# Kernel optimization log

Hardware: AMD Instinct MI355X
Metric: run time of the kernel (lower is better)

Reference implementation:

```python
import jax, jax.numpy as jnp
import numpy as np

ALPHA = 0.2   # LeakyReLU slope
V = 7         # graph nodes (hard-coded 7x7 adjacency in source)
BN_EPS = 1e-5


def _leaky(x):
    return jnp.where(x >= 0, x, ALPHA * x)


def _norm_adj(B):
    # adj = min-max normalized (B + I), then D^{-1/2} adj D^{-1/2}
    adj = B + jnp.eye(V, dtype=B.dtype)
    adj = (adj - adj.min()) / (adj.max() - adj.min())
    inv = 1.0 / jnp.sqrt(jnp.sum(adj, axis=1))
    return adj * inv[:, None] * inv[None, :]


def _gat1_head(h_flat, W, a, B):
    # h_flat: (N, V, C*T)=  (N,7,180); W: (180,9); a: (18,1); B: (7,7)
    Wh = h_flat @ W                       # (N, V, E)
    E = W.shape[1]
    s_i = Wh @ a[:E, 0]                   # (N, V)  == [Wh_i ; .] part of concat score
    s_j = Wh @ a[E:, 0]                   # (N, V)  == [. ; Wh_j] part
    e = _leaky(s_i[:, :, None] + s_j[:, None, :])   # (N, V, V)
    att = jax.nn.softmax(e, axis=-1)
    adjn = _norm_adj(B)
    att = jnp.einsum('ik,nkj->nij', adjn, att)      # adj_norm @ attention
    return jax.nn.elu(att @ Wh)           # (N, V, E)


def _gat2_head(h, W, a, B):
    # h: (N, V, C, 30); W: (30,10); a: (20,1); B: (7,7)
    Wh = h @ W                            # (N, V, C, F)
    F = W.shape[1]
    s_i = jnp.einsum('nvcf,f->nvc', Wh, a[:F, 0])
    s_j = jnp.einsum('nvcf,f->nvc', Wh, a[F:, 0])
    e = _leaky(s_i[:, :, None, :] + s_j[:, None, :, :])   # (N, V, V, C)
    att = jax.nn.softmax(e, axis=-1)      # softmax over channel dim (as in source)
    # nested V-loop with diag_embed == weighted sum over j, per-channel scaling
    h2 = jnp.einsum('njcf,nijc->ncfi', Wh, att)           # (N, C, F, V)
    adjn = _norm_adj(B)
    out = jnp.einsum('ncfu,uv->ncfv', h2, adjn)
    return jax.nn.elu(out)                # (N, C, F, V)


def setup_inputs() -> dict:
    key = jax.random.key(0)
    ks = jax.random.split(key, 16)
    N, C, T = 32768, 6, 30
    f32 = jnp.float32
    inp = {
        'x': jax.random.normal(ks[0], (N, C, T, V), f32),
        'bn_gamma': jax.random.uniform(ks[1], (42,), f32, 0.5, 1.5),
        'bn_beta': 0.1 * jax.random.normal(ks[2], (42,), f32),
        'W1': 0.1 * jax.random.normal(ks[3], (20, 180, 9), f32),
        'a1': 0.1 * jax.random.normal(ks[4], (20, 18, 1), f32),
        'B1': 0.01 * jax.random.uniform(ks[5], (20, V, V), f32) + 1e-6,
        'W2': 0.1 * jax.random.normal(ks[6], (3, 30, 10), f32),
        'a2': 0.1 * jax.random.normal(ks[7], (3, 20, 1), f32),
        'B2': 0.01 * jax.random.uniform(ks[8], (3, V, V), f32) + 1e-6,
        'W_ih': 0.1 * jax.random.normal(ks[9], (84, 84), f32),
        'W_hh': 0.1 * jax.random.normal(ks[10], (84, 21), f32),
        'b_ih': 0.1 * jax.random.normal(ks[11], (84,), f32),
        'b_hh': 0.1 * jax.random.normal(ks[12], (84,), f32),
        'W_out': 0.1 * jax.random.normal(ks[13], (7, 21), f32),
        'b_out': 0.1 * jax.random.normal(ks[14], (7,), f32),
    }
    return inp


def reference(x, bn_gamma, bn_beta, W1, a1, B1, W2, a2, B2,
              W_ih, W_hh, b_ih, b_hh, W_out, b_out):
    N, C, T, _ = x.shape                  # (N, 6, 30, 7)
    # data_bn: BatchNorm1d(42) in train mode (batch stats over N and T)
    xb = jnp.transpose(x, (0, 3, 1, 2)).reshape(N, V * C, T)
    mean = jnp.mean(xb, axis=(0, 2), keepdims=True)
    var = jnp.var(xb, axis=(0, 2), keepdims=True)
    xb = (xb - mean) / jnp.sqrt(var + BN_EPS)
    xb = xb * bn_gamma[None, :, None] + bn_beta[None, :, None]
    x0 = jnp.transpose(xb.reshape(N, V, C, T), (0, 2, 3, 1))   # (N, C, T, V)

    # l1: 20-head GAT on flattened (C*T) node features
    h_flat = jnp.transpose(x0, (0, 3, 1, 2)).reshape(N, V, C * T)
    heads1 = jax.vmap(_gat1_head, in_axes=(None, 0, 0, 0))(h_flat, W1, a1, B1)  # (20,N,V,9)
    x1 = jnp.moveaxis(heads1, 0, 2).reshape(N, V, C * T)       # cat over heads, last dim
    x1 = jnp.transpose(x1.reshape(N, V, C, T), (0, 2, 3, 1))   # (N, C, T, V)

    # l2: 3-head 2D GAT over the T axis
    h2in = jnp.transpose(x0, (0, 3, 1, 2))                      # (N, V, C, T)
    heads2 = jax.vmap(_gat2_head, in_axes=(None, 0, 0, 0))(h2in, W2, a2, B2)  # (3,N,C,10,V)
    x2 = jnp.moveaxis(heads2, 0, 2).reshape(N, C, 30, V)        # cat over heads on dim=2

    xcat = jnp.concatenate([x1, x2], axis=1)                    # (N, 12, 30, 7)

    # RNN head: source takes r_out[:, 0, :], so only LSTM step 0 (h0=c0=0) matters
    xs = jnp.transpose(xcat, (0, 2, 1, 3)).reshape(N, T, 84)
    gates = xs[:, 0, :] @ W_ih.T + b_ih + b_hh                  # h0=0 => W_hh term vanishes
    i_g, f_g, g_g, o_g = jnp.split(gates, 4, axis=-1)           # torch gate order i,f,g,o
    c1 = jax.nn.sigmoid(i_g) * jnp.tanh(g_g)
    h1 = jax.nn.sigmoid(o_g) * jnp.tanh(c1)
    return h1 @ W_out.T + b_out                                 # (N, 7)
```

## Files before the change

### kernel.cpp

```cpp
#include <hip/hip_runtime.h>

#define F1260 1260

__device__ __forceinline__ float leakyf(float x) { return x >= 0.f ? x : 0.2f * x; }
__device__ __forceinline__ float eluf(float x) { return x > 0.f ? x : expm1f(x); }
__device__ __forceinline__ float sigmoidf(float x) { return 1.f / (1.f + __expf(-x)); }
__device__ __forceinline__ float tanh_fast(float x) { return 1.f - 2.f / (__expf(2.f * x) + 1.f); }


__global__ __launch_bounds__(320) void kA_stats(const float* __restrict__ x,
                                                float* __restrict__ ws, int rows) {
    __shared__ float fs[1260], fq[1260];
    const int t = threadIdx.x;
    const int n0 = blockIdx.x * rows;
    if (t < 315) {
        const int f0 = t * 4;
        float s0 = 0.f, s1 = 0.f, s2 = 0.f, s3 = 0.f;
        float q0 = 0.f, q1 = 0.f, q2 = 0.f, q3 = 0.f;
#pragma unroll 16
        for (int i = 0; i < rows; ++i) {
            const float4 a = *(const float4*)(x + (size_t)(n0 + i) * F1260 + f0);
            s0 += a.x; q0 += a.x * a.x;
            s1 += a.y; q1 += a.y * a.y;
            s2 += a.z; q2 += a.z * a.z;
            s3 += a.w; q3 += a.w * a.w;
        }
        fs[f0 + 0] = s0; fq[f0 + 0] = q0;
        fs[f0 + 1] = s1; fq[f0 + 1] = q1;
        fs[f0 + 2] = s2; fq[f0 + 2] = q2;
        fs[f0 + 3] = s3; fq[f0 + 3] = q3;
    }
    __syncthreads();
    if (t < 42) {
        const int v = t / 6, c = t % 6;
        float s = 0.f, q = 0.f;
#pragma unroll
        for (int tt = 0; tt < 30; ++tt) {
            const int f = c * 210 + tt * 7 + v;
            s += fs[f];
            q += fq[f];
        }
        atomicAdd(&ws[t], s);
        atomicAdd(&ws[42 + t], q);
    }
}

__global__ __launch_bounds__(256) void kB_setup(
        const float* __restrict__ bn_gamma, const float* __restrict__ bn_beta,
        const float* __restrict__ W1, const float* __restrict__ a1, const float* __restrict__ B1,
        const float* __restrict__ W2, const float* __restrict__ a2, const float* __restrict__ B2,
        const float* __restrict__ b_ih, const float* __restrict__ b_hh,
        const float* __restrict__ W_out, const float* __restrict__ b_out,
        float* __restrict__ ws, int N) {
    const int t = threadIdx.x;
    float* pb = ws + 128;
    const int HH[6] = {0, 3, 6, 10, 13, 16};
    const int EH[6] = {0, 3, 6, 0, 3, 6};

    if (t < 42) {
        const float cnt = 30.f * (float)N;
        const float mean = ws[t] / cnt;
        const float var = ws[42 + t] / cnt - mean * mean;
        const float sc = bn_gamma[t] * rsqrtf(var + 1e-5f);
        pb[t] = sc;
        pb[64 + t] = bn_beta[t] - mean * sc;
    }
    if (t >= 64 && t < 71) {
        const int idx = t - 64;
        const float* Bp = (idx < 6) ? (B1 + HH[idx] * 49) : B2;
        float* op = pb + 128 + idx * 49;
        float adj[49];
        for (int i = 0; i < 49; ++i) adj[i] = Bp[i];
        for (int i = 0; i < 7; ++i) adj[i * 8] += 1.f;
        float mn = adj[0], mx = adj[0];
        for (int i = 1; i < 49; ++i) { mn = fminf(mn, adj[i]); mx = fmaxf(mx, adj[i]); }
        const float inv = 1.f / (mx - mn);
        float rinv[7];
        for (int i = 0; i < 7; ++i) {
            float rs = 0.f;
            for (int j = 0; j < 7; ++j) { adj[i * 7 + j] = (adj[i * 7 + j] - mn) * inv; rs += adj[i * 7 + j]; }
            rinv[i] = rsqrtf(rs);
        }
        for (int i = 0; i < 7; ++i)
            for (int j = 0; j < 7; ++j)
                op[i * 7 + j] = adj[i * 7 + j] * rinv[i] * rinv[j];
    }
    for (int task = t; task < 6 * 180; task += 256) {
        const int hh = task / 180, k = task % 180;
        const int h = HH[hh];
        const float* Wp = W1 + ((size_t)h * 180 + k) * 9;
        float si = 0.f, sj = 0.f;
        for (int e = 0; e < 9; ++e) {
            const float w = Wp[e];
            si += w * a1[h * 18 + e];
            sj += w * a1[h * 18 + 9 + e];
        }
        pb[512 + k * 21 + hh * 3 + 0] = si;
        pb[512 + k * 21 + hh * 3 + 1] = sj;
        pb[512 + k * 21 + hh * 3 + 2] = Wp[EH[hh]];
    }
    if (t < 30) {
        const float* Wp = W2 + t * 10;
        float si = 0.f, sj = 0.f;
        for (int f = 0; f < 10; ++f) {
            const float w = Wp[f];
            si += w * a2[f];
            sj += w * a2[10 + f];
        }
        for (int c = 0; c < 6; ++c) {
            const int k = c * 30 + t;
            pb[512 + k * 21 + 18] = si;
            pb[512 + k * 21 + 19] = sj;
            pb[512 + k * 21 + 20] = Wp[0];
        }
    }
    if (t < 84) pb[4832 + t] = b_ih[t] + b_hh[t];
    if (t < 147) pb[4928 + t] = W_out[t];
    if (t < 7) pb[5078 + t] = b_out[t];
}

#define RS 252
__global__ __launch_bounds__(128) void kC_main(const float* __restrict__ x,
        const float* __restrict__ pb, const float* __restrict__ Wih,
        float* __restrict__ outp, int N) {
    __shared__ __align__(16) float sm[4459];
    float* res  = sm;
    float* scsh = sm + 4032;
    float* adjL = sm + 4116;

    const int t = threadIdx.x;
    const int n0 = blockIdx.x * 16;
    const int v = (t >> 3) & 7;
    const int nl = ((t >> 6) << 3) + (t & 7);

    for (int i = t; i < 84; i += 128) scsh[i] = pb[i < 42 ? i : 22 + i];
    for (int i = t; i < 343; i += 128) adjL[i] = pb[128 + i];
    __syncthreads();

    if (v < 7) {
        float s1[18];
#pragma unroll
        for (int i = 0; i < 18; ++i) s1[i] = 0.f;
        const float* xb = x + (size_t)(n0 + nl) * F1260 + v;
        const float* WB = pb + 512;
        for (int c = 0; c < 6; ++c) {
            const float sc = scsh[v * 6 + c];
            const float sh = scsh[42 + v * 6 + c];
            const float* xr = xb + c * 210;
            const float* wb = WB + (c * 30) * 21;
            float xv[30];
#pragma unroll
            for (int tt = 0; tt < 30; ++tt) xv[tt] = xr[tt * 7];
            float g0 = 0.f, g1 = 0.f, g2 = 0.f;
#pragma unroll
            for (int tt = 0; tt < 30; ++tt) {
                const float a = xv[tt] * sc + sh;
                const float* w = wb + tt * 21;
#pragma unroll
                for (int q = 0; q < 18; ++q) s1[q] += a * w[q];
                g0 += a * w[18];
                g1 += a * w[19];
                g2 += a * w[20];
            }
            float* rp = res + nl * RS + 126 + (v * 6 + c) * 3;
            rp[0] = g0; rp[1] = g1; rp[2] = g2;
        }
#pragma unroll
        for (int q = 0; q < 18; ++q)
            res[nl * RS + v * 18 + q] = s1[q];
    }
    __syncthreads();

    const int hh = v;
    float si[7], sj[7], we[7];
#pragma unroll
    for (int vv = 0; vv < 7; ++vv) {
        const float* rp = res + nl * RS + vv * 18 + hh * 3;
        si[vv] = rp[0]; sj[vv] = rp[1]; we[vv] = rp[2];
    }
    __syncthreads();
    if (hh < 6) {
        float mxsj = sj[0];
#pragma unroll
        for (int j = 1; j < 7; ++j) mxsj = fmaxf(mxsj, sj[j]);
        float p[7];
#pragma unroll
        for (int i = 0; i < 7; ++i) {
            const float m = leakyf(si[i] + mxsj);
            float den = 0.f, num = 0.f;
#pragma unroll
            for (int j = 0; j < 7; ++j) {
                const float w = __expf(leakyf(si[i] + sj[j]) - m);
                den += w;
                num += w * we[j];
            }
            p[i] = num / den;
        }
        const float* An = adjL + hh * 49;
#pragma unroll
        for (int i = 0; i < 7; ++i) {
            float r = 0.f;
#pragma unroll
            for (int k = 0; k < 7; ++k) r += An[i * 7 + k] * p[k];
            res[nl * RS + hh * 7 + i] = eluf(r);
        }
    }
    if (v < 7) {
        const int i = v;
        float si2[6];
#pragma unroll
        for (int c = 0; c < 6; ++c)
            si2[c] = res[nl * RS + 126 + (i * 6 + c) * 3];
        float hc[6];
#pragma unroll
        for (int c = 0; c < 6; ++c) hc[c] = 0.f;
#pragma unroll
        for (int j = 0; j < 7; ++j) {
            float s[6];
            float m = -1e30f;
#pragma unroll
            for (int c = 0; c < 6; ++c) {
                const float* rp = res + nl * RS + 126 + (j * 6 + c) * 3;
                s[c] = leakyf(si2[c] + rp[1]);
                m = fmaxf(m, s[c]);
            }
            float den = 0.f;
#pragma unroll
            for (int c = 0; c < 6; ++c) { s[c] = __expf(s[c] - m); den += s[c]; }
            const float rd = 1.f / den;
#pragma unroll
            for (int c = 0; c < 6; ++c) {
                const float wh0 = res[nl * RS + 126 + (j * 6 + c) * 3 + 2];
                hc[c] += wh0 * s[c] * rd;
            }
        }
#pragma unroll
        for (int c = 0; c < 6; ++c)
            res[nl * RS + 84 + i * 6 + c] = hc[c];
    }
    __syncthreads();

    if (v < 6) {
        const int c = v;
        const float* An2 = adjL + 6 * 49;
        float h[7];
#pragma unroll
        for (int u = 0; u < 7; ++u) h[u] = res[nl * RS + 84 + u * 6 + c];
#pragma unroll
        for (int vv = 0; vv < 7; ++vv) {
            float r = 0.f;
#pragma unroll
            for (int u = 0; u < 7; ++u) r += h[u] * An2[u * 7 + vv];
            res[nl * RS + 42 + c * 7 + vv] = eluf(r);
        }
    }
    __syncthreads();

    {
        const int g8 = v;
        const float* bias = pb + 4832;
        const float4* xs4 = (const float4*)(res + nl * RS);
        for (int gi = g8; gi < 21; gi += 8) {
            float ga = bias[gi], gg = bias[42 + gi], go = bias[63 + gi];
            const float4* wa = (const float4*)(Wih + gi * 84);
            const float4* wg = (const float4*)(Wih + (42 + gi) * 84);
            const float4* wo = (const float4*)(Wih + (63 + gi) * 84);
#pragma unroll
            for (int k = 0; k < 21; ++k) {
                const float4 xv = xs4[k];
                const float4 a4 = wa[k];
                const float4 g4 = wg[k];
                const float4 o4 = wo[k];
                ga += xv.x * a4.x + xv.y * a4.y + xv.z * a4.z + xv.w * a4.w;
                gg += xv.x * g4.x + xv.y * g4.y + xv.z * g4.z + xv.w * g4.w;
                go += xv.x * o4.x + xv.y * o4.y + xv.z * o4.z + xv.w * o4.w;
            }
            const float c1 = sigmoidf(ga) * tanh_fast(gg);
            res[nl * RS + 126 + gi] = sigmoidf(go) * tanh_fast(c1);
        }
    }
    __syncthreads();

    if (t < 112) {
        const int n5 = t / 7, j = t - n5 * 7;
        const float* Wout = pb + 4928;
        float r = pb[5078 + j];
#pragma unroll
        for (int m = 0; m < 21; ++m) r += res[n5 * RS + 126 + m] * Wout[j * 21 + m];
        outp[(size_t)n0 * 7 + t] = r;
    }
}

extern "C" void kernel_launch(void* const* d_in, const int* in_sizes, int n_in,
                              void* d_out, int out_size, void* d_ws, size_t ws_size,
                              hipStream_t stream) {
    const int N = in_sizes[0] / F1260;

    const float* x        = (const float*)d_in[0];
    const float* bn_gamma = (const float*)d_in[1];
    const float* bn_beta  = (const float*)d_in[2];
    const float* W1       = (const float*)d_in[3];
    const float* a1       = (const float*)d_in[4];
    const float* B1       = (const float*)d_in[5];
    const float* W2       = (const float*)d_in[6];
    const float* a2       = (const float*)d_in[7];
    const float* B2       = (const float*)d_in[8];
    const float* W_ih     = (const float*)d_in[9];
    const float* b_ih     = (const float*)d_in[11];
    const float* b_hh     = (const float*)d_in[12];
    const float* W_out    = (const float*)d_in[13];
    const float* b_out    = (const float*)d_in[14];

    float* wsf = (float*)d_ws;

    hipMemsetAsync(d_ws, 0, 128 * sizeof(float), stream);

    kA_stats<<<dim3(256), dim3(320), 0, stream>>>(x, wsf, N / 256);
    kB_setup<<<dim3(1), dim3(256), 0, stream>>>(bn_gamma, bn_beta, W1, a1, B1,
                                                W2, a2, B2, b_ih, b_hh,
                                                W_out, b_out, wsf, N);
    kC_main<<<dim3(N / 16), dim3(128), 0, stream>>>(x, wsf + 128, W_ih, (float*)d_out, N);
}
```

Baseline: 339.5 us.

## Write transposed copy of x in stats pass for vectorized loads in main kernel

The stats kernel now also writes a padded, per-node transposed copy of x (stride 1344) into workspace while it reads x for batch-norm sums. The main kernel then loads each (v,c) time series with contiguous float4 reads instead of stride-7 scalar gathers. This costs an extra full-size write of x plus a re-read from workspace, and the path only runs when the workspace is large enough.

```diff
diff --git a/kernel.cpp b/kernel.cpp
--- a/kernel.cpp
+++ b/kernel.cpp
@@ -1,6 +1,8 @@
 #include <hip/hip_runtime.h>
 
 #define F1260 1260
+#define XT_STRIDE 1344
+#define XT_OFF 8192
 
 __device__ __forceinline__ float leakyf(float x) { return x >= 0.f ? x : 0.2f * x; }
 __device__ __forceinline__ float eluf(float x) { return x > 0.f ? x : expm1f(x); }
@@ -8,23 +10,38 @@
 __device__ __forceinline__ float tanh_fast(float x) { return 1.f - 2.f / (__expf(2.f * x) + 1.f); }
 
 
-__global__ __launch_bounds__(320) void kA_stats(const float* __restrict__ x,
-                                                float* __restrict__ ws, int rows) {
+__global__ __launch_bounds__(384) void kA_stats(const float* __restrict__ x,
+        float* __restrict__ ws, float* __restrict__ xT, int rows, int doT) {
     __shared__ float fs[1260], fq[1260];
     const int t = threadIdx.x;
     const int n0 = blockIdx.x * rows;
-    if (t < 315) {
-        const int f0 = t * 4;
-        float s0 = 0.f, s1 = 0.f, s2 = 0.f, s3 = 0.f;
-        float q0 = 0.f, q1 = 0.f, q2 = 0.f, q3 = 0.f;
-#pragma unroll 16
-        for (int i = 0; i < rows; ++i) {
-            const float4 a = *(const float4*)(x + (size_t)(n0 + i) * F1260 + f0);
+    const int f0 = t * 4;
+    const int o = t * 4;
+    const int vb = o / 192, rb = o % 192, cb = rb >> 5, t0 = rb & 31;
+    const int sbase = cb * 210 + t0 * 7 + vb;
+    const bool pz = (t0 + 2) < 30, pw = (t0 + 3) < 30;
+
+    float s0 = 0.f, s1 = 0.f, s2 = 0.f, s3 = 0.f;
+    float q0 = 0.f, q1 = 0.f, q2 = 0.f, q3 = 0.f;
+    for (int i = 0; i < rows; ++i) {
+        const float* xr = x + (size_t)(n0 + i) * F1260;
+        if (t < 315) {
+            const float4 a = *(const float4*)(xr + f0);
             s0 += a.x; q0 += a.x * a.x;
             s1 += a.y; q1 += a.y * a.y;
             s2 += a.z; q2 += a.z * a.z;
             s3 += a.w; q3 += a.w * a.w;
         }
+        if (doT && t < 336) {
+            float4 w;
+            w.x = xr[sbase];
+            w.y = xr[sbase + 7];
+            w.z = pz ? xr[sbase + 14] : 0.f;
+            w.w = pw ? xr[sbase + 21] : 0.f;
+            *(float4*)(xT + (size_t)(n0 + i) * XT_STRIDE + o) = w;
+        }
+    }
+    if (t < 315) {
         fs[f0 + 0] = s0; fq[f0 + 0] = q0;
         fs[f0 + 1] = s1; fq[f0 + 1] = q1;
         fs[f0 + 2] = s2; fq[f0 + 2] = q2;
@@ -121,8 +138,8 @@
 
 #define RS 252
 __global__ __launch_bounds__(128) void kC_main(const float* __restrict__ x,
-        const float* __restrict__ pb, const float* __restrict__ Wih,
-        float* __restrict__ outp, int N) {
+        const float* __restrict__ xT, const float* __restrict__ pb,
+        const float* __restrict__ Wih, float* __restrict__ outp, int N, int doT) {
     __shared__ __align__(16) float sm[4459];
     float* res  = sm;
     float* scsh = sm + 4032;
@@ -141,16 +158,24 @@
         float s1[18];
 #pragma unroll
         for (int i = 0; i < 18; ++i) s1[i] = 0.f;
-        const float* xb = x + (size_t)(n0 + nl) * F1260 + v;
         const float* WB = pb + 512;
+        const float* xtb = xT + (size_t)(n0 + nl) * XT_STRIDE + v * 192;
+        const float* xb  = x + (size_t)(n0 + nl) * F1260 + v;
         for (int c = 0; c < 6; ++c) {
             const float sc = scsh[v * 6 + c];
             const float sh = scsh[42 + v * 6 + c];
-            const float* xr = xb + c * 210;
             const float* wb = WB + (c * 30) * 21;
-            float xv[30];
-#pragma unroll
-            for (int tt = 0; tt < 30; ++tt) xv[tt] = xr[tt * 7];
+            float xv[32];
+            if (doT) {
+                const float4* src = (const float4*)(xtb + c * 32);
+#pragma unroll
+                for (int k = 0; k < 8; ++k)
+                    *(float4*)(xv + 4 * k) = src[k];
+            } else {
+                const float* xr = xb + c * 210;
+#pragma unroll
+                for (int tt = 0; tt < 30; ++tt) xv[tt] = xr[tt * 7];
+            }
             float g0 = 0.f, g1 = 0.f, g2 = 0.f;
 #pragma unroll
             for (int tt = 0; tt < 30; ++tt) {
@@ -313,11 +338,15 @@
 
     float* wsf = (float*)d_ws;
 
+    const int doT = (ws_size >= (size_t)(XT_OFF + (size_t)N * XT_STRIDE) * sizeof(float)) ? 1 : 0;
+    float* xT = wsf + XT_OFF;
+
     hipMemsetAsync(d_ws, 0, 128 * sizeof(float), stream);
 
-    kA_stats<<<dim3(256), dim3(320), 0, stream>>>(x, wsf, N / 256);
+    kA_stats<<<dim3(256), dim3(384), 0, stream>>>(x, wsf, xT, N / 256, doT);
     kB_setup<<<dim3(1), dim3(256), 0, stream>>>(bn_gamma, bn_beta, W1, a1, B1,
                                                 W2, a2, B2, b_ih, b_hh,
                                                 W_out, b_out, wsf, N);
-    kC_main<<<dim3(N / 16), dim3(128), 0, stream>>>(x, wsf + 128, W_ih, (float*)d_out, N);
+    kC_main<<<dim3(N / 16), dim3(128), 0, stream>>>(x, xT, wsf + 128, W_ih,
+                                                    (float*)d_out, N, doT);
 }
```

New measurement: 608.6 us. +79.3%, slower.
